# Optimization experiments

Measured on AMD Instinct MI355X. Metric: run time of the kernel, lower is better.

Reference implementation:

```python
import jax, jax.numpy as jnp
import numpy as np

N = 50000      # nodes
E = 800000     # edges
IN = 128       # in_channels
HID = 128      # hidden_channels
OUT = 40       # out_channels (classes)
L = 2          # num_layers
K = 3          # K_order
H = 1          # num_heads
EPS = 1e-5     # BatchNorm eps


def setup_inputs() -> dict:
    key = jax.random.key(0)
    ks = jax.random.split(key, 10)
    x = jax.random.normal(ks[0], (N, IN), jnp.float32)
    edge_index = jax.random.randint(ks[1], (2, E), 0, N, dtype=jnp.int32)
    def lin(k, sh, fan):
        return jax.random.normal(k, sh, jnp.float32) / np.float32(np.sqrt(fan))
    W_in = lin(ks[2], (IN, HID), IN); b_in = jnp.zeros((HID,), jnp.float32)
    Wq = lin(ks[3], (L, HID, HID * H), HID); bq = jnp.zeros((L, HID * H), jnp.float32)
    Wk = lin(ks[4], (L, HID, HID * H), HID); bk = jnp.zeros((L, HID * H), jnp.float32)
    fc_in = HID * (K + H + 1)  # 640: cat of attn (HID*H) and gnn (HID*(K+1))
    Wfc = lin(ks[5], (L, fc_in, HID), fc_in); bfc = jnp.zeros((L, HID), jnp.float32)
    W_out = lin(ks[6], (HID, OUT), HID); b_out = jnp.zeros((OUT,), jnp.float32)
    bn_g = jnp.ones((L + 1, HID), jnp.float32)
    bn_b = jnp.zeros((L + 1, HID), jnp.float32)
    return dict(x=x, edge_index=edge_index, W_in=W_in, b_in=b_in, Wq=Wq, bq=bq,
                Wk=Wk, bk=bk, Wfc=Wfc, bfc=bfc, W_out=W_out, b_out=b_out,
                bn_g=bn_g, bn_b=bn_b)


def _bn(x, g, b):
    # BatchNorm1d with batch statistics (biased variance), affine params g, b
    m = x.mean(axis=0)
    v = ((x - m) ** 2).mean(axis=0)
    return g * (x - m) * jax.lax.rsqrt(v + EPS) + b


def reference(x, edge_index, W_in, b_in, Wq, bq, Wk, bk, Wfc, bfc, W_out, b_out, bn_g, bn_b):
    row, col = edge_index[0], edge_index[1]
    # symmetric-normalized adjacency: A_hat[col,row] = d[col]^-1/2 * d[row]^-1/2
    deg = jax.ops.segment_sum(jnp.ones((E,), x.dtype), col, num_segments=N)
    dis = jnp.where(deg > 0, deg ** -0.5, 0.0)
    ew = dis[col] * dis[row]  # [E]

    def prop(h):  # out[c] = sum_e ew[e] * h[row[e]] scattered to col[e]
        return jax.ops.segment_sum(ew[:, None] * h[row], col, num_segments=N)

    h = jax.nn.relu(_bn(x @ W_in + b_in, bn_g[0], bn_b[0]))
    for i in range(L):
        # --- global linear attention (kernel='simple', non-blockwise) ---
        q = (h @ Wq[i] + bq[i]).reshape(N, H, HID)
        k = (h @ Wk[i] + bk[i]).reshape(N, H, HID)
        v = jnp.broadcast_to(h[:, None, :], (N, H, HID))
        qn = q / jnp.linalg.norm(q, axis=2, keepdims=True)
        kn = k / jnp.linalg.norm(k, axis=2, keepdims=True)
        kvs = jnp.einsum('lhm,lhd->hmd', kn, v)                 # [H,D,D]
        num = jnp.einsum('nhm,hmd->nhd', qn, kvs) + v.sum(0)    # [N,H,D]
        den = jnp.einsum('nhm,hm->nh', qn, kn.sum(0))[..., None] + jnp.asarray(N, x.dtype)
        x1 = (num / den).reshape(N, H * HID)
        # --- K-hop normalized-adjacency diffusion ---
        xs = [h]
        for _ in range(K):
            xs.append(prop(xs[-1]))
        x2 = jnp.concatenate(xs, axis=1)                         # [N, HID*(K+1)]
        z = jnp.concatenate([x1, x2], axis=1) @ Wfc[i] + bfc[i]
        z = z + h  # residual
        h = jax.nn.relu(_bn(z, bn_g[i + 1], bn_b[i + 1]))
    return h @ W_out + b_out
```

## Files before the change

kernel.cpp:

```cpp
#include <hip/hip_runtime.h>
#include <hip/hip_bf16.h>
#include <hip/hip_fp16.h>
#include <math.h>

#define NN 50000
#define NE 800000
#define HD 128
#define EPS_BN 1e-5f

typedef __bf16 bf16_t;
typedef bf16_t bf16x8 __attribute__((ext_vector_type(8)));
typedef bf16_t bf16x4 __attribute__((ext_vector_type(4)));
typedef float f32x4 __attribute__((ext_vector_type(4)));

__global__ void count_edges(const int* __restrict__ col, int* __restrict__ counts, int E) {
    int e = blockIdx.x * 256 + threadIdx.x;
    if (e >= E) return;
    atomicAdd(&counts[col[e]], 1);
}

__global__ __launch_bounds__(256) void scan1(const int* __restrict__ counts,
                                             int* __restrict__ offsets,
                                             int* __restrict__ bsum,
                                             float* __restrict__ dis, int n) {
    __shared__ int wsl[4];
    int t = threadIdx.x, lane = t & 63, w = t >> 6;
    int i = blockIdx.x * 256 + t;
    int v = (i < n) ? counts[i] : 0;
    if (i < n) dis[i] = (v > 0) ? rsqrtf((float)v) : 0.0f;
    int x = v;
    #pragma unroll
    for (int o = 1; o < 64; o <<= 1) {
        int tt = __shfl_up(x, o, 64);
        if (lane >= o) x += tt;
    }
    if (lane == 63) wsl[w] = x;
    __syncthreads();
    if (t == 0) {
        int s = 0;
        #pragma unroll
        for (int k = 0; k < 4; k++) { int tmp = wsl[k]; wsl[k] = s; s += tmp; }
        bsum[blockIdx.x] = s;
    }
    __syncthreads();
    if (i < n) offsets[i] = x - v + wsl[w];
}

__global__ __launch_bounds__(256) void scan2(int* __restrict__ bsum, int* __restrict__ offsets,
                                             int nb, int n) {
    __shared__ int wsl[4];
    int t = threadIdx.x, lane = t & 63, w = t >> 6;
    int v = (t < nb) ? bsum[t] : 0;
    int x = v;
    #pragma unroll
    for (int o = 1; o < 64; o <<= 1) {
        int tt = __shfl_up(x, o, 64);
        if (lane >= o) x += tt;
    }
    if (lane == 63) wsl[w] = x;
    __syncthreads();
    if (t == 0) {
        int s = 0;
        #pragma unroll
        for (int k = 0; k < 4; k++) { int tmp = wsl[k]; wsl[k] = s; s += tmp; }
    }
    __syncthreads();
    int excl = x - v + wsl[w];
    if (t < nb) bsum[t] = excl;
    if (t == nb - 1) offsets[n] = excl + v;
}

__global__ void scan3(int* __restrict__ offsets, const int* __restrict__ bsum, int n) {
    int i = blockIdx.x * 256 + threadIdx.x;
    if (i < n) offsets[i] += bsum[blockIdx.x];
}

__global__ void scatter_edges3(const int* __restrict__ row, const int* __restrict__ col,
                               const float* __restrict__ dis, const int* __restrict__ offsets,
                               int* __restrict__ cursor, unsigned int* __restrict__ edges,
                               int E) {
    int e = blockIdx.x * 256 + threadIdx.x;
    if (e >= E) return;
    int c = col[e], r = row[e];
    int pos = offsets[c] + atomicAdd(&cursor[c], 1);
    unsigned short hw = __half_as_ushort(__float2half(dis[c] * dis[r]));
    edges[pos] = (unsigned int)r | ((unsigned int)hw << 16);
}

__global__ __launch_bounds__(256) void prop_b3(const int* __restrict__ offsets,
                                               const unsigned int* __restrict__ edges,
                                               const bf16_t* __restrict__ in,
                                               bf16_t* __restrict__ out) {
    int wave = threadIdx.x >> 6;
    int lane = threadIdx.x & 63;
    int q = lane >> 4;
    int ch8 = (lane & 15) * 8;
    int c = blockIdx.x * 4 + wave;
    if (c >= NN) return;
    int s = offsets[c], e = offsets[c + 1];
    float a[8] = {};
    int i = s + q;
    for (; i + 4 < e; i += 8) {
        unsigned int r0 = edges[i], r1 = edges[i + 4];
        bf16x8 v0 = *(const bf16x8*)(in + ((size_t)(r0 & 0xFFFFu) << 7) + ch8);
        bf16x8 v1 = *(const bf16x8*)(in + ((size_t)(r1 & 0xFFFFu) << 7) + ch8);
        float w0 = __half2float(__ushort_as_half((unsigned short)(r0 >> 16)));
        float w1 = __half2float(__ushort_as_half((unsigned short)(r1 >> 16)));
        #pragma unroll
        for (int j = 0; j < 8; j++) a[j] += w0 * (float)v0[j] + w1 * (float)v1[j];
    }
    for (; i < e; i += 4) {
        unsigned int r0 = edges[i];
        bf16x8 v0 = *(const bf16x8*)(in + ((size_t)(r0 & 0xFFFFu) << 7) + ch8);
        float w0 = __half2float(__ushort_as_half((unsigned short)(r0 >> 16)));
        #pragma unroll
        for (int j = 0; j < 8; j++) a[j] += w0 * (float)v0[j];
    }
    #pragma unroll
    for (int j = 0; j < 8; j++) {
        a[j] += __shfl_xor(a[j], 16);
        a[j] += __shfl_xor(a[j], 32);
    }
    if (q == 0) {
        bf16x8 o;
        #pragma unroll
        for (int j = 0; j < 8; j++) o[j] = (bf16_t)a[j];
        *(bf16x8*)(out + ((size_t)c << 7) + ch8) = o;
    }
}

__device__ inline void pack_frag(const float* __restrict__ W, bf16_t* __restrict__ Wp, int nkc,
                                 int lb) {
    int p = lb * 256 + threadIdx.x;
    if (p >= 8 * nkc * 64) return;
    int lane = p & 63;
    int tk = p >> 6;
    int kc = tk % nkc;
    int t = tk / nkc;
    int n = t * 16 + (lane & 15);
    int k0 = kc * 32 + (lane >> 4) * 8;
    bf16x8 f;
    #pragma unroll
    for (int j = 0; j < 8; j++) f[j] = (bf16_t)W[(size_t)(k0 + j) * 128 + n];
    *(bf16x8*)(Wp + (size_t)p * 8) = f;
}

__global__ void wcvt_all(const float* __restrict__ W_in, const float* __restrict__ Wq,
                         const float* __restrict__ Wk, const float* __restrict__ Wfc,
                         const float* __restrict__ W_out, bf16_t* __restrict__ Wp_in,
                         bf16_t* __restrict__ Wp_q, bf16_t* __restrict__ Wp_k,
                         bf16_t* __restrict__ Wp_fc, bf16_t* __restrict__ Wp_out,
                         float* __restrict__ bnsum, float* __restrict__ bnsumsq) {
    const int QSZ = HD * HD;
    const int FSZ = 8 * 20 * 64 * 8;
    int b = blockIdx.x;
    if (b < 8) { pack_frag(W_in, Wp_in, 4, b); return; }
    if (b < 16) { pack_frag(Wq, Wp_q, 4, b - 8); return; }
    if (b < 24) { pack_frag(Wq + QSZ, Wp_q + QSZ, 4, b - 16); return; }
    if (b < 32) { pack_frag(Wk, Wp_k, 4, b - 24); return; }
    if (b < 40) { pack_frag(Wk + QSZ, Wp_k + QSZ, 4, b - 32); return; }
    if (b < 80) { pack_frag(Wfc, Wp_fc, 20, b - 40); return; }
    if (b < 120) { pack_frag(Wfc + 640 * HD, Wp_fc + FSZ, 20, b - 80); return; }
    if (b < 123) {
        int p = (b - 120) * 256 + threadIdx.x;
        if (p >= 3 * 4 * 64) return;
        int lane = p & 63;
        int tk = p >> 6;
        int kc = tk & 3;
        int t = tk >> 2;
        int n = t * 16 + (lane & 15);
        int k0 = kc * 32 + (lane >> 4) * 8;
        bf16x8 f;
        #pragma unroll
        for (int j = 0; j < 8; j++)
            f[j] = (n < 40) ? (bf16_t)W_out[(size_t)(k0 + j) * 40 + n] : (bf16_t)0.0f;
        *(bf16x8*)(Wp_out + (size_t)p * 8) = f;
        return;
    }
    int t = threadIdx.x;
    if (t < 128) bnsum[t] = 0.0f;
    else bnsumsq[t - 128] = 0.0f;
}

__device__ inline bf16x8 loadA(const float* ap) {
    float4 a0 = *(const float4*)ap;
    float4 a1 = *(const float4*)(ap + 4);
    bf16x8 f;
    f[0] = (bf16_t)a0.x; f[1] = (bf16_t)a0.y; f[2] = (bf16_t)a0.z; f[3] = (bf16_t)a0.w;
    f[4] = (bf16_t)a1.x; f[5] = (bf16_t)a1.y; f[6] = (bf16_t)a1.z; f[7] = (bf16_t)a1.w;
    return f;
}
__device__ inline bf16x8 loadA(const bf16_t* ap) { return *(const bf16x8*)ap; }

template <typename T, bool NORM>
__global__ __launch_bounds__(256) void gemm128s(const T* __restrict__ A,
                                                const bf16_t* __restrict__ Wp,
                                                const float* __restrict__ bias,
                                                const float* __restrict__ ksum_p,
                                                float* __restrict__ den_out,
                                                float* __restrict__ sums,
                                                float* __restrict__ sumsq,
                                                float* __restrict__ zero_buf, int zero_len,
                                                float* __restrict__ out,
                                                bf16_t* __restrict__ outb, int N) {
    __shared__ float lsum[128], lsq[128];
    int tid = threadIdx.x;
    if (zero_buf && blockIdx.x < 17) {
        int base = (blockIdx.x * 256 + tid) * 4;
        if (base < zero_len) *(float4*)(zero_buf + base) = make_float4(0.f, 0.f, 0.f, 0.f);
    }
    int wave = tid >> 6;
    int lane = tid & 63;
    int quad = lane >> 4;
    int l16 = lane & 15;
    int m0 = blockIdx.x * 64 + wave * 16;
    int arow = m0 + l16;

    bf16x8 afr[4];
    if (arow < N) {
        #pragma unroll
        for (int kc = 0; kc < 4; kc++)
            afr[kc] = loadA(A + ((size_t)arow << 7) + kc * 32 + quad * 8);
    } else {
        #pragma unroll
        for (int kc = 0; kc < 4; kc++) afr[kc] = (bf16x8){};
    }

    f32x4 acc[8] = {};
    #pragma unroll
    for (int kc = 0; kc < 4; kc++) {
        bf16x8 bfr[8];
        #pragma unroll
        for (int t = 0; t < 8; t++)
            bfr[t] = *(const bf16x8*)(Wp + (size_t)(((t * 4 + kc) * 64) + lane) * 8);
        #pragma unroll
        for (int t = 0; t < 8; t++)
            acc[t] = __builtin_amdgcn_mfma_f32_16x16x32_bf16(afr[kc], bfr[t], acc[t], 0, 0, 0);
    }
    float vals[8][4];
    #pragma unroll
    for (int t = 0; t < 8; t++) {
        float b = bias ? bias[t * 16 + l16] : 0.0f;
        #pragma unroll
        for (int r = 0; r < 4; r++) vals[t][r] = acc[t][r] + b;
    }
    if (NORM) {
        #pragma unroll
        for (int r = 0; r < 4; r++) {
            float p = 0.0f;
            #pragma unroll
            for (int t = 0; t < 8; t++) p += vals[t][r] * vals[t][r];
            p += __shfl_xor(p, 1);
            p += __shfl_xor(p, 2);
            p += __shfl_xor(p, 4);
            p += __shfl_xor(p, 8);
            float inv = rsqrtf(p);
            #pragma unroll
            for (int t = 0; t < 8; t++) vals[t][r] *= inv;
        }
    }
    if (ksum_p) {
        float kv[8];
        #pragma unroll
        for (int t = 0; t < 8; t++) kv[t] = ksum_p[t * 16 + l16];
        #pragma unroll
        for (int r = 0; r < 4; r++) {
            float dp = 0.0f;
            #pragma unroll
            for (int t = 0; t < 8; t++) dp += vals[t][r] * kv[t];
            dp += __shfl_xor(dp, 1);
            dp += __shfl_xor(dp, 2);
            dp += __shfl_xor(dp, 4);
            dp += __shfl_xor(dp, 8);
            float dv = dp + (float)NN;
            int rr = m0 + quad * 4 + r;
            if (l16 == 0 && rr < N) den_out[rr] = dv;
            float dinv = 1.0f / dv;
            #pragma unroll
            for (int t = 0; t < 8; t++) vals[t][r] *= dinv;
        }
    }
    #pragma unroll
    for (int r = 0; r < 4; r++) {
        int rr = m0 + quad * 4 + r;
        if (rr >= N) continue;
        #pragma unroll
        for (int t = 0; t < 8; t++) {
            int c = t * 16 + l16;
            float v = vals[t][r];
            if (out) out[((size_t)rr << 7) + c] = v;
            if (outb) outb[((size_t)rr << 7) + c] = (bf16_t)v;
        }
    }
    if (sums) {
        if (tid < 128) { lsum[tid] = 0.0f; lsq[tid] = 0.0f; }
        __syncthreads();
        float sp[8] = {}, qp[8] = {};
        #pragma unroll
        for (int r = 0; r < 4; r++) {
            int rr = m0 + quad * 4 + r;
            if (rr >= N) continue;
            #pragma unroll
            for (int t = 0; t < 8; t++) {
                float v = vals[t][r];
                sp[t] += v;
                qp[t] += v * v;
            }
        }
        #pragma unroll
        for (int t = 0; t < 8; t++) {
            sp[t] += __shfl_xor(sp[t], 16);
            sp[t] += __shfl_xor(sp[t], 32);
            qp[t] += __shfl_xor(qp[t], 16);
            qp[t] += __shfl_xor(qp[t], 32);
        }
        if (quad == 0) {
            #pragma unroll
            for (int t = 0; t < 8; t++) {
                atomicAdd(&lsum[t * 16 + l16], sp[t]);
                atomicAdd(&lsq[t * 16 + l16], qp[t]);
            }
        }
        __syncthreads();
        if (tid < 128) {
            atomicAdd(&sums[tid], lsum[tid]);
            atomicAdd(&sumsq[tid], lsq[tid]);
        }
    }
}

__global__ __launch_bounds__(256, 1) void gemm_fc(
    const bf16_t* __restrict__ qn, const bf16_t* __restrict__ s1, const bf16_t* __restrict__ s2,
    const bf16_t* __restrict__ s3, const bf16_t* __restrict__ s4,
    const bf16_t* __restrict__ WpM1, const bf16_t* __restrict__ Wp,
    const float* __restrict__ bvec, const float* __restrict__ bfc,
    const float* __restrict__ den, const bf16_t* __restrict__ resb,
    float* __restrict__ sums, float* __restrict__ sumsq,
    bf16_t* __restrict__ outb, int N) {
    __shared__ float lsum[128], lsq[128];
    const bf16_t* srcs[5] = {qn, s1, s2, s3, s4};
    int tid = threadIdx.x;
    int wave = tid >> 6;
    int lane = tid & 63;
    int quad = lane >> 4;
    int l16 = lane & 15;
    int m0 = blockIdx.x * 128 + wave * 32;

    f32x4 acc[2][8] = {};
    #pragma unroll
    for (int kc = 0; kc < 20; kc++) {
        int s = kc >> 2;
        int klocal = (kc & 3) * 32;
        bf16x8 bfr[8];
        #pragma unroll
        for (int t = 0; t < 8; t++) {
            const bf16_t* bp = (kc < 4) ? WpM1 + (size_t)(((t * 4 + kc) * 64) + lane) * 8
                                        : Wp + (size_t)(((t * 20 + kc) * 64) + lane) * 8;
            bfr[t] = *(const bf16x8*)bp;
        }
        bf16x8 af[2] = {};
        #pragma unroll
        for (int m = 0; m < 2; m++) {
            int arow = m0 + m * 16 + l16;
            if (arow < N)
                af[m] = *(const bf16x8*)(srcs[s] + ((size_t)arow << 7) + klocal + quad * 8);
        }
        #pragma unroll
        for (int t = 0; t < 8; t++) {
            #pragma unroll
            for (int m = 0; m < 2; m++)
                acc[m][t] = __builtin_amdgcn_mfma_f32_16x16x32_bf16(af[m], bfr[t], acc[m][t],
                                                                    0, 0, 0);
        }
    }
    float bv[8], bf[8];
    #pragma unroll
    for (int t = 0; t < 8; t++) {
        bv[t] = bvec[t * 16 + l16];
        bf[t] = bfc[t * 16 + l16];
    }
    if (tid < 128) { lsum[tid] = 0.0f; lsq[tid] = 0.0f; }
    __syncthreads();
    float sp[8] = {}, qp[8] = {};
    #pragma unroll
    for (int m = 0; m < 2; m++) {
        #pragma unroll
        for (int r = 0; r < 4; r++) {
            int rr = m0 + m * 16 + quad * 4 + r;
            if (rr >= N) continue;
            float dinv = 1.0f / den[rr];
            #pragma unroll
            for (int t = 0; t < 8; t++) {
                int c = t * 16 + l16;
                float v = acc[m][t][r] + dinv * bv[t] + bf[t] +
                          (float)resb[((size_t)rr << 7) + c];
                outb[((size_t)rr << 7) + c] = (bf16_t)v;
                sp[t] += v;
                qp[t] += v * v;
            }
        }
    }
    #pragma unroll
    for (int t = 0; t < 8; t++) {
        sp[t] += __shfl_xor(sp[t], 16);
        sp[t] += __shfl_xor(sp[t], 32);
        qp[t] += __shfl_xor(qp[t], 16);
        qp[t] += __shfl_xor(qp[t], 32);
    }
    if (quad == 0) {
        #pragma unroll
        for (int t = 0; t < 8; t++) {
            atomicAdd(&lsum[t * 16 + l16], sp[t]);
            atomicAdd(&lsq[t * 16 + l16], qp[t]);
        }
    }
    __syncthreads();
    if (tid < 128) {
        atomicAdd(&sums[tid], lsum[tid]);
        atomicAdd(&sumsq[tid], lsq[tid]);
    }
}

__global__ __launch_bounds__(256) void out_mfma(const bf16_t* __restrict__ hb,
                                                const bf16_t* __restrict__ Wp,
                                                const float* __restrict__ bias,
                                                float* __restrict__ out, int N) {
    int wave = threadIdx.x >> 6;
    int lane = threadIdx.x & 63;
    int quad = lane >> 4;
    int l16 = lane & 15;
    int m0 = blockIdx.x * 64 + wave * 16;
    int arow = m0 + l16;

    bf16x8 afr[4];
    if (arow < N) {
        #pragma unroll
        for (int kc = 0; kc < 4; kc++)
            afr[kc] = *(const bf16x8*)(hb + ((size_t)arow << 7) + kc * 32 + quad * 8);
    } else {
        #pragma unroll
        for (int kc = 0; kc < 4; kc++) afr[kc] = (bf16x8){};
    }
    f32x4 acc[3] = {};
    #pragma unroll
    for (int kc = 0; kc < 4; kc++) {
        #pragma unroll
        for (int t = 0; t < 3; t++) {
            const bf16_t* bp = Wp + (size_t)(((t * 4 + kc) * 64) + lane) * 8;
            acc[t] = __builtin_amdgcn_mfma_f32_16x16x32_bf16(afr[kc], *(const bf16x8*)bp,
                                                             acc[t], 0, 0, 0);
        }
    }
    #pragma unroll
    for (int r = 0; r < 4; r++) {
        int rr = m0 + quad * 4 + r;
        if (rr >= N) continue;
        #pragma unroll
        for (int t = 0; t < 3; t++) {
            int c = t * 16 + l16;
            if (c < 40) out[(size_t)rr * 40 + c] = acc[t][r] + bias[c];
        }
    }
}

__global__ __launch_bounds__(256) void kvs_mfma(const bf16_t* __restrict__ kn,
                                                const bf16_t* __restrict__ v,
                                                float* __restrict__ kvs,
                                                float* __restrict__ ksum,
                                                float* __restrict__ vsum, int N) {
    __shared__ bf16_t Lk[32][132];
    __shared__ bf16_t Lv[32][132];
    __shared__ float lred[256];
    int t = threadIdx.x;
    int wave = t >> 6, lane = t & 63, quad = lane >> 4, l16 = lane & 15;
    int tr = t >> 4, tc = (t & 15) * 8;
    int mbase = wave * 32;
    f32x4 acc[2][8] = {};
    float ks[8] = {}, vs[8] = {};
    for (int base = blockIdx.x * 32; base < N; base += gridDim.x * 32) {
        __syncthreads();
        #pragma unroll
        for (int hh = 0; hh < 2; hh++) {
            int r = hh * 16 + tr;
            int rowi = base + r;
            bf16x8 ck = {}, cv = {};
            if (rowi < N) {
                ck = *(const bf16x8*)(kn + ((size_t)rowi << 7) + tc);
                cv = *(const bf16x8*)(v + ((size_t)rowi << 7) + tc);
            }
            bf16x4 klo, khi, vlo, vhi;
            #pragma unroll
            for (int j = 0; j < 4; j++) {
                klo[j] = ck[j]; khi[j] = ck[j + 4];
                vlo[j] = cv[j]; vhi[j] = cv[j + 4];
                ks[j] += (float)ck[j]; ks[j + 4] += (float)ck[j + 4];
                vs[j] += (float)cv[j]; vs[j + 4] += (float)cv[j + 4];
            }
            *(bf16x4*)&Lk[r][tc] = klo;
            *(bf16x4*)&Lk[r][tc + 4] = khi;
            *(bf16x4*)&Lv[r][tc] = vlo;
            *(bf16x4*)&Lv[r][tc + 4] = vhi;
        }
        __syncthreads();
        bf16x8 af[2], bfr[8];
        #pragma unroll
        for (int mt = 0; mt < 2; mt++)
            #pragma unroll
            for (int j = 0; j < 8; j++) af[mt][j] = Lk[quad * 8 + j][mbase + mt * 16 + l16];
        #pragma unroll
        for (int tt = 0; tt < 8; tt++)
            #pragma unroll
            for (int j = 0; j < 8; j++) bfr[tt][j] = Lv[quad * 8 + j][tt * 16 + l16];
        #pragma unroll
        for (int mt = 0; mt < 2; mt++)
            #pragma unroll
            for (int tt = 0; tt < 8; tt++)
                acc[mt][tt] = __builtin_amdgcn_mfma_f32_16x16x32_bf16(af[mt], bfr[tt],
                                                                      acc[mt][tt], 0, 0, 0);
    }
    #pragma unroll
    for (int mt = 0; mt < 2; mt++)
        #pragma unroll
        for (int tt = 0; tt < 8; tt++)
            #pragma unroll
            for (int r = 0; r < 4; r++) {
                int m = mbase + mt * 16 + quad * 4 + r;
                int d = tt * 16 + l16;
                atomicAdd(&kvs[m * HD + d], acc[mt][tt][r]);
            }
    lred[t] = 0.0f;
    __syncthreads();
    #pragma unroll
    for (int j = 0; j < 8; j++) {
        atomicAdd(&lred[tc + j], ks[j]);
        atomicAdd(&lred[128 + tc + j], vs[j]);
    }
    __syncthreads();
    if (t < 128) {
        atomicAdd(&ksum[t], lred[t]);
        atomicAdd(&vsum[t], lred[t + 128]);
    }
}

__global__ void m1_pack(const float* __restrict__ kvs, const float* __restrict__ W0,
                        const float* __restrict__ vsum, bf16_t* __restrict__ WpM1,
                        float* __restrict__ bvec, float* __restrict__ bnsum,
                        float* __restrict__ bnsumsq) {
    if (blockIdx.x == 64) {
        int t = threadIdx.x;
        if (t < 128) {
            bnsum[t] = 0.0f;
            float acc = 0.0f;
            for (int d = 0; d < 128; d++) acc += vsum[d] * W0[d * 128 + t];
            bvec[t] = acc;
        } else {
            bnsumsq[t - 128] = 0.0f;
        }
        return;
    }
    int idx = blockIdx.x * 256 + threadIdx.x;
    int m = idx >> 7;
    int c = idx & 127;
    float acc = 0.0f;
    for (int d = 0; d < 128; d += 4) {
        float4 k4 = *(const float4*)(kvs + m * 128 + d);
        acc += k4.x * W0[(d + 0) * 128 + c] + k4.y * W0[(d + 1) * 128 + c] +
               k4.z * W0[(d + 2) * 128 + c] + k4.w * W0[(d + 3) * 128 + c];
    }
    int t = c >> 4, l16 = c & 15, kc = m >> 5, quad = (m >> 3) & 3, j = m & 7;
    int lane = quad * 16 + l16;
    WpM1[(size_t)(((t * 4 + kc) * 64) + lane) * 8 + j] = (bf16_t)acc;
}

__global__ void bn_apply2(const bf16_t* __restrict__ z, bf16_t* __restrict__ hb,
                          const float* __restrict__ sums, const float* __restrict__ sumsq,
                          const float* __restrict__ g, const float* __restrict__ bb, int n4) {
    __shared__ float sc[128], sh[128];
    int t = threadIdx.x;
    if (t < 128) {
        float m = sums[t] / (float)NN;
        float var = sumsq[t] / (float)NN - m * m;
        float s = g[t] * rsqrtf(var + EPS_BN);
        sc[t] = s;
        sh[t] = bb[t] - m * s;
    }
    __syncthreads();
    int i = blockIdx.x * 256 + t;
    if (i >= n4) return;
    int c4 = (i & 31) * 4;
    bf16x4 zv = *(const bf16x4*)(z + (size_t)i * 4);
    bf16x4 o;
    #pragma unroll
    for (int j = 0; j < 4; j++)
        o[j] = (bf16_t)fmaxf((float)zv[j] * sc[c4 + j] + sh[c4 + j], 0.0f);
    *(bf16x4*)(hb + (size_t)i * 4) = o;
}

extern "C" void kernel_launch(void* const* d_in, const int* in_sizes, int n_in,
                              void* d_out, int out_size, void* d_ws, size_t ws_size,
                              hipStream_t stream) {
    const float* x = (const float*)d_in[0];
    const int* eidx = (const int*)d_in[1];
    const float* W_in = (const float*)d_in[2];
    const float* b_in = (const float*)d_in[3];
    const float* Wq = (const float*)d_in[4];
    const float* bq = (const float*)d_in[5];
    const float* Wk = (const float*)d_in[6];
    const float* bk = (const float*)d_in[7];
    const float* Wfc = (const float*)d_in[8];
    const float* bfc = (const float*)d_in[9];
    const float* W_out = (const float*)d_in[10];
    const float* b_out = (const float*)d_in[11];
    const float* bn_g = (const float*)d_in[12];
    const float* bn_b = (const float*)d_in[13];
    float* out = (float*)d_out;

    const int N = NN, E = NE;
    const int* rowp = eidx;
    const int* colp = eidx + E;

    char* ws = (char*)d_ws;
    size_t off = 0;
    auto nxt = [&](size_t bytes) -> void* {
        void* p = ws + off;
        off += (bytes + 255) & ~(size_t)255;
        return p;
    };
    int* counts = (int*)nxt((size_t)N * 4);
    int* cursor = (int*)nxt((size_t)N * 4);
    int* offsets = (int*)nxt((size_t)(N + 1) * 4);
    int* bsum = (int*)nxt(1024);
    unsigned int* edges = (unsigned int*)nxt((size_t)E * 4);
    float* dis = (float*)nxt((size_t)N * 4);
    float* den = (float*)nxt((size_t)N * 4);
    float* kvs = (float*)nxt((size_t)HD * HD * 4);
    float* ksum = (float*)nxt((size_t)HD * 4);
    float* vsum = (float*)nxt((size_t)HD * 4);
    float* bnsum = (float*)nxt((size_t)HD * 4);
    float* bnsumsq = (float*)nxt((size_t)HD * 4);
    float* bvec = (float*)nxt((size_t)HD * 4);
    bf16_t* zb = (bf16_t*)nxt((size_t)N * HD * 2);
    bf16_t* hb = (bf16_t*)nxt((size_t)N * HD * 2);
    bf16_t* p1b = (bf16_t*)nxt((size_t)N * HD * 2);
    bf16_t* p2b = (bf16_t*)nxt((size_t)N * HD * 2);
    bf16_t* p3b = (bf16_t*)nxt((size_t)N * HD * 2);
    bf16_t* knb = (bf16_t*)nxt((size_t)N * HD * 2);
    bf16_t* qnb = (bf16_t*)nxt((size_t)N * HD * 2);
    bf16_t* Wp_in = (bf16_t*)nxt((size_t)8 * 4 * 64 * 8 * 2);
    bf16_t* Wp_q = (bf16_t*)nxt((size_t)2 * 8 * 4 * 64 * 8 * 2);
    bf16_t* Wp_k = (bf16_t*)nxt((size_t)2 * 8 * 4 * 64 * 8 * 2);
    bf16_t* Wp_fc = (bf16_t*)nxt((size_t)2 * 8 * 20 * 64 * 8 * 2);
    bf16_t* WpM1 = (bf16_t*)nxt((size_t)8 * 4 * 64 * 8 * 2);
    bf16_t* Wp_out = (bf16_t*)nxt((size_t)3 * 4 * 64 * 8 * 2);

    const int GB = (N + 63) / 64;
    const int GB2 = (N + 127) / 128;
    const int QSZ = HD * HD;
    const int FSZ = 8 * 20 * 64 * 8;
    const int NB = (N + 255) / 256;

    hipMemsetAsync(counts, 0, (size_t)2 * ((N * 4 + 255) & ~255), stream);
    count_edges<<<(E + 255) / 256, 256, 0, stream>>>(colp, counts, E);
    scan1<<<NB, 256, 0, stream>>>(counts, offsets, bsum, dis, N);
    scan2<<<1, 256, 0, stream>>>(bsum, offsets, NB, N);
    scan3<<<NB, 256, 0, stream>>>(offsets, bsum, N);
    scatter_edges3<<<(E + 255) / 256, 256, 0, stream>>>(rowp, colp, dis, offsets, cursor,
                                                        edges, E);

    wcvt_all<<<124, 256, 0, stream>>>(W_in, Wq, Wk, Wfc, W_out, Wp_in, Wp_q, Wp_k, Wp_fc,
                                      Wp_out, bnsum, bnsumsq);

    gemm128s<float, false><<<GB, 256, 0, stream>>>(x, Wp_in, b_in, nullptr, nullptr, bnsum,
                                                   bnsumsq, nullptr, 0, nullptr, zb, N);
    bn_apply2<<<(N * 32 + 255) / 256, 256, 0, stream>>>(zb, hb, bnsum, bnsumsq, bn_g, bn_b,
                                                        N * 32);

    for (int i = 0; i < 2; i++) {
        const float* bq_i = bq + (size_t)i * HD;
        const float* bk_i = bk + (size_t)i * HD;
        const float* bfc_i = bfc + (size_t)i * HD;
        const float* Wfc_i = Wfc + (size_t)i * 640 * HD;
        bf16_t* Wp_q_i = Wp_q + (size_t)i * QSZ;
        bf16_t* Wp_k_i = Wp_k + (size_t)i * QSZ;
        bf16_t* Wp_fc_i = Wp_fc + (size_t)i * FSZ;

        prop_b3<<<(N + 3) / 4, 256, 0, stream>>>(offsets, edges, hb, p1b);
        prop_b3<<<(N + 3) / 4, 256, 0, stream>>>(offsets, edges, p1b, p2b);
        prop_b3<<<(N + 3) / 4, 256, 0, stream>>>(offsets, edges, p2b, p3b);

        gemm128s<bf16_t, true><<<GB, 256, 0, stream>>>(hb, Wp_k_i, bk_i, nullptr, nullptr,
                                                       nullptr, nullptr, kvs, HD * HD + 2 * HD,
                                                       nullptr, knb, N);
        kvs_mfma<<<256, 256, 0, stream>>>(knb, hb, kvs, ksum, vsum, N);
        gemm128s<bf16_t, true><<<GB, 256, 0, stream>>>(hb, Wp_q_i, bq_i, ksum, den, nullptr,
                                                       nullptr, nullptr, 0, nullptr, qnb, N);
        m1_pack<<<65, 256, 0, stream>>>(kvs, Wfc_i, vsum, WpM1, bvec, bnsum, bnsumsq);

        gemm_fc<<<GB2, 256, 0, stream>>>(qnb, hb, p1b, p2b, p3b, WpM1, Wp_fc_i, bvec, bfc_i,
                                         den, hb, bnsum, bnsumsq, zb, N);
        bn_apply2<<<(N * 32 + 255) / 256, 256, 0, stream>>>(zb, hb, bnsum, bnsumsq,
                                                            bn_g + (size_t)(i + 1) * HD,
                                                            bn_b + (size_t)(i + 1) * HD,
                                                            N * 32);
    }

    out_mfma<<<GB, 256, 0, stream>>>(hb, Wp_out, b_out, out, N);
}
```

Baseline: 611.4 us.

## Double rows per wave in gemm128s, prefetch edges in prop, nontemporal edge stores

gemm128s now processes two 16-row tiles per wave, so each block covers 128 rows and reuses each loaded weight fragment across two MFMAs. Its launch grids drop to GB2 and launch bounds are set to one block per SM. prop_b3 software-pipelines the edge-index loads by fetching the next pair before the current gathers, and its tail loop is replaced by a single conditional step. scatter_edges3 writes edge records with nontemporal stores. The wider tile doubles accumulator registers and halves the block count, which may lower occupancy and latency hiding.

```diff
diff --git a/kernel.cpp b/kernel.cpp
--- a/kernel.cpp
+++ b/kernel.cpp
@@ -84,7 +84,8 @@
     int c = col[e], r = row[e];
     int pos = offsets[c] + atomicAdd(&cursor[c], 1);
     unsigned short hw = __half_as_ushort(__float2half(dis[c] * dis[r]));
-    edges[pos] = (unsigned int)r | ((unsigned int)hw << 16);
+    unsigned int rec = (unsigned int)r | ((unsigned int)hw << 16);
+    __builtin_nontemporal_store(rec, &edges[pos]);
 }
 
 __global__ __launch_bounds__(256) void prop_b3(const int* __restrict__ offsets,
@@ -100,19 +101,25 @@
     int s = offsets[c], e = offsets[c + 1];
     float a[8] = {};
     int i = s + q;
-    for (; i + 4 < e; i += 8) {
-        unsigned int r0 = edges[i], r1 = edges[i + 4];
+    int last = (e > 0) ? e - 1 : 0;
+    unsigned int n0 = edges[(i < e) ? i : last];
+    unsigned int n1 = edges[(i + 4 < e) ? i + 4 : last];
+    while (i + 4 < e) {
+        unsigned int r0 = n0, r1 = n1;
+        int inext = i + 8;
+        n0 = edges[(inext < e) ? inext : last];
+        n1 = edges[(inext + 4 < e) ? inext + 4 : last];
         bf16x8 v0 = *(const bf16x8*)(in + ((size_t)(r0 & 0xFFFFu) << 7) + ch8);
         bf16x8 v1 = *(const bf16x8*)(in + ((size_t)(r1 & 0xFFFFu) << 7) + ch8);
         float w0 = __half2float(__ushort_as_half((unsigned short)(r0 >> 16)));
         float w1 = __half2float(__ushort_as_half((unsigned short)(r1 >> 16)));
         #pragma unroll
         for (int j = 0; j < 8; j++) a[j] += w0 * (float)v0[j] + w1 * (float)v1[j];
-    }
-    for (; i < e; i += 4) {
-        unsigned int r0 = edges[i];
-        bf16x8 v0 = *(const bf16x8*)(in + ((size_t)(r0 & 0xFFFFu) << 7) + ch8);
-        float w0 = __half2float(__ushort_as_half((unsigned short)(r0 >> 16)));
+        i = inext;
+    }
+    if (i < e) {
+        bf16x8 v0 = *(const bf16x8*)(in + ((size_t)(n0 & 0xFFFFu) << 7) + ch8);
+        float w0 = __half2float(__ushort_as_half((unsigned short)(n0 >> 16)));
         #pragma unroll
         for (int j = 0; j < 8; j++) a[j] += w0 * (float)v0[j];
     }
@@ -193,16 +200,16 @@
 __device__ inline bf16x8 loadA(const bf16_t* ap) { return *(const bf16x8*)ap; }
 
 template <typename T, bool NORM>
-__global__ __launch_bounds__(256) void gemm128s(const T* __restrict__ A,
-                                                const bf16_t* __restrict__ Wp,
-                                                const float* __restrict__ bias,
-                                                const float* __restrict__ ksum_p,
-                                                float* __restrict__ den_out,
-                                                float* __restrict__ sums,
-                                                float* __restrict__ sumsq,
-                                                float* __restrict__ zero_buf, int zero_len,
-                                                float* __restrict__ out,
-                                                bf16_t* __restrict__ outb, int N) {
+__global__ __launch_bounds__(256, 1) void gemm128s(const T* __restrict__ A,
+                                                   const bf16_t* __restrict__ Wp,
+                                                   const float* __restrict__ bias,
+                                                   const float* __restrict__ ksum_p,
+                                                   float* __restrict__ den_out,
+                                                   float* __restrict__ sums,
+                                                   float* __restrict__ sumsq,
+                                                   float* __restrict__ zero_buf, int zero_len,
+                                                   float* __restrict__ out,
+                                                   bf16_t* __restrict__ outb, int N) {
     __shared__ float lsum[128], lsq[128];
     int tid = threadIdx.x;
     if (zero_buf && blockIdx.x < 17) {
@@ -213,20 +220,23 @@
     int lane = tid & 63;
     int quad = lane >> 4;
     int l16 = lane & 15;
-    int m0 = blockIdx.x * 64 + wave * 16;
-    int arow = m0 + l16;
-
-    bf16x8 afr[4];
-    if (arow < N) {
-        #pragma unroll
-        for (int kc = 0; kc < 4; kc++)
-            afr[kc] = loadA(A + ((size_t)arow << 7) + kc * 32 + quad * 8);
-    } else {
-        #pragma unroll
-        for (int kc = 0; kc < 4; kc++) afr[kc] = (bf16x8){};
-    }
-
-    f32x4 acc[8] = {};
+    int m0 = blockIdx.x * 128 + wave * 32;
+
+    bf16x8 afr[2][4];
+    #pragma unroll
+    for (int m = 0; m < 2; m++) {
+        int arow = m0 + m * 16 + l16;
+        if (arow < N) {
+            #pragma unroll
+            for (int kc = 0; kc < 4; kc++)
+                afr[m][kc] = loadA(A + ((size_t)arow << 7) + kc * 32 + quad * 8);
+        } else {
+            #pragma unroll
+            for (int kc = 0; kc < 4; kc++) afr[m][kc] = (bf16x8){};
+        }
+    }
+
+    f32x4 acc[2][8] = {};
     #pragma unroll
     for (int kc = 0; kc < 4; kc++) {
         bf16x8 bfr[8];
@@ -235,61 +245,66 @@
             bfr[t] = *(const bf16x8*)(Wp + (size_t)(((t * 4 + kc) * 64) + lane) * 8);
         #pragma unroll
         for (int t = 0; t < 8; t++)
-            acc[t] = __builtin_amdgcn_mfma_f32_16x16x32_bf16(afr[kc], bfr[t], acc[t], 0, 0, 0);
-    }
-    float vals[8][4];
-    #pragma unroll
-    for (int t = 0; t < 8; t++) {
-        float b = bias ? bias[t * 16 + l16] : 0.0f;
-        #pragma unroll
-        for (int r = 0; r < 4; r++) vals[t][r] = acc[t][r] + b;
-    }
-    if (NORM) {
+            #pragma unroll
+            for (int m = 0; m < 2; m++)
+                acc[m][t] = __builtin_amdgcn_mfma_f32_16x16x32_bf16(afr[m][kc], bfr[t],
+                                                                    acc[m][t], 0, 0, 0);
+    }
+    #pragma unroll
+    for (int m = 0; m < 2; m++) {
+        #pragma unroll
+        for (int t = 0; t < 8; t++) {
+            float b = bias ? bias[t * 16 + l16] : 0.0f;
+            #pragma unroll
+            for (int r = 0; r < 4; r++) acc[m][t][r] += b;
+        }
+        if (NORM) {
+            #pragma unroll
+            for (int r = 0; r < 4; r++) {
+                float p = 0.0f;
+                #pragma unroll
+                for (int t = 0; t < 8; t++) p += acc[m][t][r] * acc[m][t][r];
+                p += __shfl_xor(p, 1);
+                p += __shfl_xor(p, 2);
+                p += __shfl_xor(p, 4);
+                p += __shfl_xor(p, 8);
+                float inv = rsqrtf(p);
+                #pragma unroll
+                for (int t = 0; t < 8; t++) acc[m][t][r] *= inv;
+            }
+        }
+        if (ksum_p) {
+            float kv[8];
+            #pragma unroll
+            for (int t = 0; t < 8; t++) kv[t] = ksum_p[t * 16 + l16];
+            #pragma unroll
+            for (int r = 0; r < 4; r++) {
+                float dp = 0.0f;
+                #pragma unroll
+                for (int t = 0; t < 8; t++) dp += acc[m][t][r] * kv[t];
+                dp += __shfl_xor(dp, 1);
+                dp += __shfl_xor(dp, 2);
+                dp += __shfl_xor(dp, 4);
+                dp += __shfl_xor(dp, 8);
+                float dv = dp + (float)NN;
+                int rr = m0 + m * 16 + quad * 4 + r;
+                if (l16 == 0 && rr < N) den_out[rr] = dv;
+                float dinv = 1.0f / dv;
+                #pragma unroll
+                for (int t = 0; t < 8; t++) acc[m][t][r] *= dinv;
+            }
+        }
         #pragma unroll
         for (int r = 0; r < 4; r++) {
-            float p = 0.0f;
-            #pragma unroll
-            for (int t = 0; t < 8; t++) p += vals[t][r] * vals[t][r];
-            p += __shfl_xor(p, 1);
-            p += __shfl_xor(p, 2);
-            p += __shfl_xor(p, 4);
-            p += __shfl_xor(p, 8);
-            float inv = rsqrtf(p);
-            #pragma unroll
-            for (int t = 0; t < 8; t++) vals[t][r] *= inv;
-        }
-    }
-    if (ksum_p) {
-        float kv[8];
-        #pragma unroll
-        for (int t = 0; t < 8; t++) kv[t] = ksum_p[t * 16 + l16];
-        #pragma unroll
-        for (int r = 0; r < 4; r++) {
-            float dp = 0.0f;
-            #pragma unroll
-            for (int t = 0; t < 8; t++) dp += vals[t][r] * kv[t];
-            dp += __shfl_xor(dp, 1);
-            dp += __shfl_xor(dp, 2);
-            dp += __shfl_xor(dp, 4);
-            dp += __shfl_xor(dp, 8);
-            float dv = dp + (float)NN;
-            int rr = m0 + quad * 4 + r;
-            if (l16 == 0 && rr < N) den_out[rr] = dv;
-            float dinv = 1.0f / dv;
-            #pragma unroll
-            for (int t = 0; t < 8; t++) vals[t][r] *= dinv;
-        }
-    }
-    #pragma unroll
-    for (int r = 0; r < 4; r++) {
-        int rr = m0 + quad * 4 + r;
-        if (rr >= N) continue;
-        #pragma unroll
-        for (int t = 0; t < 8; t++) {
-            int c = t * 16 + l16;
-            float v = vals[t][r];
-            if (out) out[((size_t)rr << 7) + c] = v;
-            if (outb) outb[((size_t)rr << 7) + c] = (bf16_t)v;
+            int rr = m0 + m * 16 + quad * 4 + r;
+            if (rr >= N) continue;
+            #pragma unroll
+            for (int t = 0; t < 8; t++) {
+                int c = t * 16 + l16;
+                float v = acc[m][t][r];
+                if (out) out[((size_t)rr << 7) + c] = v;
+                if (outb) outb[((size_t)rr << 7) + c] = (bf16_t)v;
+            }
         }
     }
     if (sums) {
@@ -297,16 +312,18 @@
         __syncthreads();
         float sp[8] = {}, qp[8] = {};
         #pragma unroll
-        for (int r = 0; r < 4; r++) {
-            int rr = m0 + quad * 4 + r;
-            if (rr >= N) continue;
-            #pragma unroll
-            for (int t = 0; t < 8; t++) {
-                float v = vals[t][r];
-                sp[t] += v;
-                qp[t] += v * v;
-            }
-        }
+        for (int m = 0; m < 2; m++)
+            #pragma unroll
+            for (int r = 0; r < 4; r++) {
+                int rr = m0 + m * 16 + quad * 4 + r;
+                if (rr >= N) continue;
+                #pragma unroll
+                for (int t = 0; t < 8; t++) {
+                    float v = acc[m][t][r];
+                    sp[t] += v;
+                    qp[t] += v * v;
+                }
+            }
         #pragma unroll
         for (int t = 0; t < 8; t++) {
             sp[t] += __shfl_xor(sp[t], 16);
@@ -670,8 +687,8 @@
     wcvt_all<<<124, 256, 0, stream>>>(W_in, Wq, Wk, Wfc, W_out, Wp_in, Wp_q, Wp_k, Wp_fc,
                                       Wp_out, bnsum, bnsumsq);
 
-    gemm128s<float, false><<<GB, 256, 0, stream>>>(x, Wp_in, b_in, nullptr, nullptr, bnsum,
-                                                   bnsumsq, nullptr, 0, nullptr, zb, N);
+    gemm128s<float, false><<<GB2, 256, 0, stream>>>(x, Wp_in, b_in, nullptr, nullptr, bnsum,
+                                                    bnsumsq, nullptr, 0, nullptr, zb, N);
     bn_apply2<<<(N * 32 + 255) / 256, 256, 0, stream>>>(zb, hb, bnsum, bnsumsq, bn_g, bn_b,
                                                         N * 32);
 
@@ -688,12 +705,12 @@
         prop_b3<<<(N + 3) / 4, 256, 0, stream>>>(offsets, edges, p1b, p2b);
         prop_b3<<<(N + 3) / 4, 256, 0, stream>>>(offsets, edges, p2b, p3b);
 
-        gemm128s<bf16_t, true><<<GB, 256, 0, stream>>>(hb, Wp_k_i, bk_i, nullptr, nullptr,
-                                                       nullptr, nullptr, kvs, HD * HD + 2 * HD,
-                                                       nullptr, knb, N);
+        gemm128s<bf16_t, true><<<GB2, 256, 0, stream>>>(hb, Wp_k_i, bk_i, nullptr, nullptr,
+                                                        nullptr, nullptr, kvs,
+                                                        HD * HD + 2 * HD, nullptr, knb, N);
         kvs_mfma<<<256, 256, 0, stream>>>(knb, hb, kvs, ksum, vsum, N);
-        gemm128s<bf16_t, true><<<GB, 256, 0, stream>>>(hb, Wp_q_i, bq_i, ksum, den, nullptr,
-                                                       nullptr, nullptr, 0, nullptr, qnb, N);
+        gemm128s<bf16_t, true><<<GB2, 256, 0, stream>>>(hb, Wp_q_i, bq_i, ksum, den, nullptr,
+                                                        nullptr, nullptr, 0, nullptr, qnb, N);
         m1_pack<<<65, 256, 0, stream>>>(kvs, Wfc_i, vsum, WpM1, bvec, bnsum, bnsumsq);
 
         gemm_fc<<<GB2, 256, 0, stream>>>(qnb, hb, p1b, p2b, p3b, WpM1, Wp_fc_i, bvec, bfc_i,
```

Result: no change. 602.8 us (-1.4%).
